# Kernel tuning notes

Hardware: AMD Instinct MI355X
Metric: run time of the kernel (lower is better)

Reference implementation:

```python
import jax, jax.numpy as jnp
import numpy as np

B, S, H = 2, 2048, 2048
N_HEADS = 16
HEAD_DIM = H // N_HEADS


def setup_inputs() -> dict:
    key = jax.random.key(0)
    k1, k2, k3 = jax.random.split(key, 3)
    # Xavier-uniform-ish init for weights, zeros for biases (matches _init_weights)
    lim_in = float(np.sqrt(6.0 / (H + 3 * H)))
    lim_out = float(np.sqrt(6.0 / (H + H)))
    return {
        "hidden_states": jax.random.normal(k1, (B, S, H), dtype=jnp.float32),
        "W_in": jax.random.uniform(k2, (3 * H, H), jnp.float32, -lim_in, lim_in),
        "b_in": jnp.zeros((3 * H,), jnp.float32),
        "W_out": jax.random.uniform(k3, (H, H), jnp.float32, -lim_out, lim_out),
        "b_out": jnp.zeros((H,), jnp.float32),
    }


def reference(hidden_states, W_in, b_in, W_out, b_out):
    b, s, h = hidden_states.shape
    qkv = hidden_states @ W_in.T + b_in  # [B,S,3H]
    q, k, v = jnp.split(qkv, 3, axis=-1)
    # [B,S,H] -> [B,N,S,D]
    def to_heads(x):
        return x.reshape(b, s, N_HEADS, HEAD_DIM).transpose(0, 2, 1, 3)
    q, k, v = to_heads(q), to_heads(k), to_heads(v)
    scale = HEAD_DIM ** -0.5
    scores = jnp.einsum("bnqd,bnkd->bnqk", q, k) * scale  # [B,N,S,S]
    causal = jnp.triu(jnp.ones((s, s), dtype=bool), k=1)
    scores = jnp.where(causal, -jnp.inf, scores)
    weights = jax.nn.softmax(scores, axis=-1)
    attn = jnp.einsum("bnqk,bnkd->bnqd", weights, v)  # [B,N,S,D]
    attn = attn.transpose(0, 2, 1, 3).reshape(b, s, h)
    return attn @ W_out.T + b_out
```

## Files before the change

kernel.cpp:

```cpp
#include <hip/hip_runtime.h>
#include <cstdint>

typedef __bf16 bf16x8 __attribute__((ext_vector_type(8)));
typedef __bf16 bf16x4 __attribute__((ext_vector_type(4)));
typedef float  f32x4  __attribute__((ext_vector_type(4)));

__device__ __forceinline__ void lds_load16(const void* g, void* l) {
  __builtin_amdgcn_global_load_lds(
      (const __attribute__((address_space(1))) unsigned int*)g,
      (__attribute__((address_space(3))) unsigned int*)l, 16, 0, 0);
}

__device__ __forceinline__ float grp16_max(float v) {
  v = fmaxf(v, __shfl_xor(v, 1));
  v = fmaxf(v, __shfl_xor(v, 2));
  v = fmaxf(v, __shfl_xor(v, 4));
  v = fmaxf(v, __shfl_xor(v, 8));
  return v;
}
__device__ __forceinline__ float grp16_sum(float v) {
  v += __shfl_xor(v, 1);
  v += __shfl_xor(v, 2);
  v += __shfl_xor(v, 4);
  v += __shfl_xor(v, 8);
  return v;
}

__global__ void f2bf_kernel(const float* __restrict__ in, __bf16* __restrict__ out, int n4) {
  int i = blockIdx.x * blockDim.x + threadIdx.x;
  if (i >= n4) return;
  const float4 v = reinterpret_cast<const float4*>(in)[i];
  bf16x4 o;
  o[0] = (__bf16)v.x; o[1] = (__bf16)v.y; o[2] = (__bf16)v.z; o[3] = (__bf16)v.w;
  reinterpret_cast<bf16x4*>(out)[i] = o;
}

template <int EPI>
__global__ __launch_bounds__(256)
void gemm_bt(const __bf16* __restrict__ A, const __bf16* __restrict__ Bm,
             int M, int N, int K, const float* __restrict__ bias,
             __bf16* __restrict__ qo, __bf16* __restrict__ ko, __bf16* __restrict__ vo,
             float* __restrict__ co)
{
  __shared__ __align__(16) __bf16 As[128 * 32];
  __shared__ __align__(16) __bf16 Bs[128 * 32];
  const int t = threadIdx.x;
  const int lane = t & 63, w = t >> 6;
  const int g = lane >> 4, r16 = lane & 15;
  const int tM = blockIdx.y * 128, tN = blockIdx.x * 128;
  const int wrow = (w >> 1) * 64, wcol = (w & 1) * 64;

  f32x4 acc[4][4] = {};
  const char* Ag = (const char*)A + (size_t)tM * K * 2;
  const char* Bg = (const char*)Bm + (size_t)tN * K * 2;
  const int ldb = K * 2;

  for (int k0 = 0; k0 < K; k0 += 32) {
    const char* Ak = Ag + (size_t)k0 * 2;
    const char* Bk = Bg + (size_t)k0 * 2;
#pragma unroll
    for (int it = 0; it < 2; it++) {
      int o = it * 4096 + t * 16;
      lds_load16(Ak + (size_t)(o >> 6) * ldb + (o & 63), (char*)As + o);
    }
#pragma unroll
    for (int it = 0; it < 2; it++) {
      int o = it * 4096 + t * 16;
      lds_load16(Bk + (size_t)(o >> 6) * ldb + (o & 63), (char*)Bs + o);
    }
    __syncthreads();
    bf16x8 af[4], bfr[4];
#pragma unroll
    for (int i = 0; i < 4; i++) af[i]  = *(const bf16x8*)&As[(wrow + i * 16 + r16) * 32 + g * 8];
#pragma unroll
    for (int i = 0; i < 4; i++) bfr[i] = *(const bf16x8*)&Bs[(wcol + i * 16 + r16) * 32 + g * 8];
#pragma unroll
    for (int i = 0; i < 4; i++)
#pragma unroll
      for (int j = 0; j < 4; j++)
        acc[i][j] = __builtin_amdgcn_mfma_f32_16x16x32_bf16(af[i], bfr[j], acc[i][j], 0, 0, 0);
    __syncthreads();
  }

  if (EPI == 0) {
#pragma unroll
    for (int j = 0; j < 4; j++) {
      int col = tN + wcol + j * 16 + r16;
      float bv = bias[col];
      int which = col >> 11;
      int f = col & 2047;
      int head = f >> 7, dd = f & 127;
      if (which == 2) {
#pragma unroll
        for (int i = 0; i < 4; i++) {
#pragma unroll
          for (int r = 0; r < 4; r++) {
            int m = tM + wrow + i * 16 + g * 4 + r;
            int bb = m >> 11, s = m & 2047;
            vo[((size_t)(bb * 16 + head) * 128 + dd) * 2048 + s] = (__bf16)(acc[i][j][r] + bv);
          }
        }
      } else {
        __bf16* dst = (which == 0) ? qo : ko;
        float sc = (which == 0) ? 0.12751757f : 1.0f;
#pragma unroll
        for (int i = 0; i < 4; i++) {
#pragma unroll
          for (int r = 0; r < 4; r++) {
            int m = tM + wrow + i * 16 + g * 4 + r;
            int bb = m >> 11, s = m & 2047;
            dst[((size_t)(bb * 16 + head) * 2048 + s) * 128 + dd] = (__bf16)((acc[i][j][r] + bv) * sc);
          }
        }
      }
    }
  } else {
#pragma unroll
    for (int j = 0; j < 4; j++) {
      int col = tN + wcol + j * 16 + r16;
      float bv = bias[col];
#pragma unroll
      for (int i = 0; i < 4; i++) {
#pragma unroll
        for (int r = 0; r < 4; r++) {
          int m = tM + wrow + i * 16 + g * 4 + r;
          co[(size_t)m * N + col] = acc[i][j][r] + bv;
        }
      }
    }
  }
}

__global__ __launch_bounds__(256)
void attn_kernel(const __bf16* __restrict__ Qb, const __bf16* __restrict__ Kb,
                 const __bf16* __restrict__ Vb, __bf16* __restrict__ Ob)
{
  const int pi = blockIdx.x;
  const int bh = blockIdx.y;
  const int b = bh >> 4, head = bh & 15;
  const int t = threadIdx.x, lane = t & 63, w = t >> 6;
  const int g = lane >> 4, r16 = lane & 15;

  __shared__ __align__(16) __bf16 Ks[2][64 * 128];
  __shared__ __align__(16) __bf16 Vs[2][128 * 64];
  __shared__ __align__(16) __bf16 Ps[4][16 * 72];

  const int qiS = pi, qiL = 31 - pi;
  const int q0S = qiS * 64, q0L = qiL * 64;

  const size_t hoff = (size_t)bh * 2048 * 128;
  const char* Kt0 = (const char*)(Kb + hoff);
  const char* Vt0 = (const char*)(Vb + hoff);

  bf16x8 qfL[4], qfS[4];
  {
    const __bf16* qp = Qb + hoff + (size_t)(q0L + w * 16 + r16) * 128 + g * 8;
#pragma unroll
    for (int ks = 0; ks < 4; ks++) qfL[ks] = *(const bf16x8*)(qp + ks * 32);
    const __bf16* qp2 = Qb + hoff + (size_t)(q0S + w * 16 + r16) * 128 + g * 8;
#pragma unroll
    for (int ks = 0; ks < 4; ks++) qfS[ks] = *(const bf16x8*)(qp2 + ks * 32);
  }

  f32x4 oL[8] = {}, oS[8] = {};
  float mL[4], lL[4], mS[4], lS[4];
#pragma unroll
  for (int r = 0; r < 4; r++) { mL[r] = -1e30f; lL[r] = 0.f; mS[r] = -1e30f; lS[r] = 0.f; }

#define STAGE(bb_, kt_) do {                                                   \
  const char* kg_ = Kt0 + (size_t)(kt_) * 16384;                               \
  const char* vg_ = Vt0 + (size_t)(kt_) * 128;                                 \
  _Pragma("unroll")                                                            \
  for (int it = 0; it < 4; it++) {                                             \
    int o = it * 4096 + t * 16;                                                \
    int swz = o ^ (((o >> 8) & 7) << 4);                                       \
    lds_load16(kg_ + swz, (char*)Ks[bb_] + o);                                 \
  }                                                                            \
  _Pragma("unroll")                                                            \
  for (int it = 0; it < 4; it++) {                                             \
    int o = it * 4096 + t * 16;                                                \
    int swz = o ^ (((o >> 7) & 7) << 4);                                       \
    lds_load16(vg_ + (size_t)(swz >> 7) * 4096 + (swz & 127), (char*)Vs[bb_] + o); \
  }                                                                            \
} while (0)

#define TILE_COMPUTE(qfX, oX, mX, lX, q0X, isDiag, bb_) do {                   \
  f32x4 sf[4];                                                                 \
  _Pragma("unroll")                                                            \
  for (int ni = 0; ni < 4; ni++) {                                             \
    f32x4 a = {};                                                              \
    _Pragma("unroll")                                                          \
    for (int ks = 0; ks < 4; ks++) {                                           \
      int row = ni * 16 + r16;                                                 \
      int off = (row * 256 + (ks * 32 + g * 8) * 2) ^ ((row & 7) << 4);        \
      bf16x8 kf = *(const bf16x8*)((const char*)Ks[bb_] + off);                \
      a = __builtin_amdgcn_mfma_f32_16x16x32_bf16(qfX[ks], kf, a, 0, 0, 0);    \
    }                                                                          \
    sf[ni] = a;                                                                \
  }                                                                            \
  if (isDiag) {                                                                \
    _Pragma("unroll")                                                          \
    for (int ni = 0; ni < 4; ni++) {                                           \
      int kg2 = kt * 64 + ni * 16 + r16;                                       \
      _Pragma("unroll")                                                        \
      for (int r = 0; r < 4; r++) {                                            \
        int qg = q0X + w * 16 + g * 4 + r;                                     \
        if (kg2 > qg) sf[ni][r] = -1e30f;                                      \
      }                                                                        \
    }                                                                          \
  }                                                                            \
  _Pragma("unroll")                                                            \
  for (int r = 0; r < 4; r++) {                                                \
    float mx = fmaxf(fmaxf(sf[0][r], sf[1][r]), fmaxf(sf[2][r], sf[3][r]));    \
    mx = grp16_max(mx);                                                        \
    float mn = fmaxf(mX[r], mx);                                               \
    float alpha = __builtin_amdgcn_exp2f(mX[r] - mn);                          \
    float ps = 0.f;                                                            \
    _Pragma("unroll")                                                          \
    for (int ni = 0; ni < 4; ni++) {                                           \
      float p = __builtin_amdgcn_exp2f(sf[ni][r] - mn);                        \
      sf[ni][r] = p; ps += p;                                                  \
    }                                                                          \
    ps = grp16_sum(ps);                                                        \
    lX[r] = lX[r] * alpha + ps;                                                \
    mX[r] = mn;                                                                \
    _Pragma("unroll")                                                          \
    for (int di = 0; di < 8; di++) oX[di][r] *= alpha;                         \
  }                                                                            \
  _Pragma("unroll")                                                            \
  for (int ni = 0; ni < 4; ni++)                                               \
    _Pragma("unroll")                                                          \
    for (int r = 0; r < 4; r++)                                                \
      Ps[w][(g * 4 + r) * 72 + ni * 16 + r16] = (__bf16)sf[ni][r];             \
  _Pragma("unroll")                                                            \
  for (int ks2 = 0; ks2 < 2; ks2++) {                                          \
    bf16x8 pa = *(const bf16x8*)&Ps[w][r16 * 72 + ks2 * 32 + g * 8];           \
    _Pragma("unroll")                                                          \
    for (int di = 0; di < 8; di++) {                                           \
      int d_ = di * 16 + r16;                                                  \
      int off = ((d_ << 7) + (ks2 * 32 + g * 8) * 2) ^ ((d_ & 7) << 4);        \
      bf16x8 vf = *(const bf16x8*)((const char*)Vs[bb_] + off);                \
      oX[di] = __builtin_amdgcn_mfma_f32_16x16x32_bf16(pa, vf, oX[di], 0, 0, 0); \
    }                                                                          \
  }                                                                            \
} while (0)

  STAGE(0, 0);
  __syncthreads();

  for (int kt = 0; kt <= qiL; ++kt) {
    const int bb = kt & 1;
    if (kt < qiL) STAGE(bb ^ 1, kt + 1);
    TILE_COMPUTE(qfL, oL, mL, lL, q0L, (kt == qiL), bb);
    if (kt <= qiS) TILE_COMPUTE(qfS, oS, mS, lS, q0S, (kt == qiS), bb);
    __syncthreads();
  }

#undef STAGE
#undef TILE_COMPUTE

#pragma unroll
  for (int r = 0; r < 4; r++) {
    float invL = 1.0f / lL[r];
    size_t rowL = ((size_t)b * 2048 + q0L + w * 16 + g * 4 + r) * 2048 + head * 128 + r16;
#pragma unroll
    for (int di = 0; di < 8; di++)
      Ob[rowL + di * 16] = (__bf16)(oL[di][r] * invL);
    float invS = 1.0f / lS[r];
    size_t rowS = ((size_t)b * 2048 + q0S + w * 16 + g * 4 + r) * 2048 + head * 128 + r16;
#pragma unroll
    for (int di = 0; di < 8; di++)
      Ob[rowS + di * 16] = (__bf16)(oS[di][r] * invS);
  }
}

extern "C" void kernel_launch(void* const* d_in, const int* in_sizes, int n_in,
                              void* d_out, int out_size, void* d_ws, size_t ws_size,
                              hipStream_t stream) {
  const float* X  = (const float*)d_in[0];
  const float* Wi = (const float*)d_in[1];
  const float* bi = (const float*)d_in[2];
  const float* Wo = (const float*)d_in[3];
  const float* bo = (const float*)d_in[4];
  float* out = (float*)d_out;

  char* p = (char*)d_ws;
  auto alloc = [&](size_t bytes) {
    char* r = p;
    p += (bytes + 255) & ~(size_t)255;
    return r;
  };
  __bf16* Xb  = (__bf16*)alloc((size_t)4096 * 2048 * 2);
  __bf16* Wib = (__bf16*)alloc((size_t)6144 * 2048 * 2);
  __bf16* Wob = (__bf16*)alloc((size_t)2048 * 2048 * 2);
  __bf16* Qb  = (__bf16*)alloc((size_t)32 * 2048 * 128 * 2);
  __bf16* Kb  = (__bf16*)alloc((size_t)32 * 2048 * 128 * 2);
  __bf16* Vb  = (__bf16*)alloc((size_t)32 * 2048 * 128 * 2);
  __bf16* Ab  = (__bf16*)alloc((size_t)4096 * 2048 * 2);

  {
    int n4 = 4096 * 2048 / 4;
    f2bf_kernel<<<(n4 + 255) / 256, 256, 0, stream>>>(X, Xb, n4);
  }
  {
    int n4 = 6144 * 2048 / 4;
    f2bf_kernel<<<(n4 + 255) / 256, 256, 0, stream>>>(Wi, Wib, n4);
  }
  {
    int n4 = 2048 * 2048 / 4;
    f2bf_kernel<<<(n4 + 255) / 256, 256, 0, stream>>>(Wo, Wob, n4);
  }

  gemm_bt<0><<<dim3(48, 32), 256, 0, stream>>>(Xb, Wib, 4096, 6144, 2048, bi,
                                               Qb, Kb, Vb, nullptr);
  attn_kernel<<<dim3(16, 32), 256, 0, stream>>>(Qb, Kb, Vb, Ab);
  gemm_bt<1><<<dim3(16, 32), 256, 0, stream>>>(Ab, Wob, 4096, 2048, 2048, bo,
                                               nullptr, nullptr, nullptr, out);
}
```

Baseline: 489.8 us.

## Add 256x256 ping-pong QKV GEMM, swizzle output GEMM LDS, raise MFMA priority

Replaces the QKV projection GEMM with a dedicated 256x256-tile kernel. It uses 512 threads, 128KB of double-buffered LDS, an XOR swizzle, split half-tile staging interleaved with MFMA phases and s_setprio, and a grouped block-index swizzle for L2 locality. The output GEMM gets an XOR swizzle on its LDS layout to reduce bank conflicts. The attention kernel raises wave priority around its MFMA sections. The aim is higher MFMA utilisation and less LDS and memory stall. The cost is more complex barrier and waitcnt logic and only one block per CU.

```diff
diff --git a/kernel.cpp b/kernel.cpp
--- a/kernel.cpp
+++ b/kernel.cpp
@@ -10,6 +10,8 @@
       (const __attribute__((address_space(1))) unsigned int*)g,
       (__attribute__((address_space(3))) unsigned int*)l, 16, 0, 0);
 }
+
+#define BAR() do { asm volatile("" ::: "memory"); __builtin_amdgcn_s_barrier(); asm volatile("" ::: "memory"); } while (0)
 
 __device__ __forceinline__ float grp16_max(float v) {
   v = fmaxf(v, __shfl_xor(v, 1));
@@ -35,12 +37,180 @@
   reinterpret_cast<bf16x4*>(out)[i] = o;
 }
 
-template <int EPI>
+__global__ __launch_bounds__(512, 1)
+void gemm256_qkv(const __bf16* __restrict__ A, const __bf16* __restrict__ Bm,
+                 const float* __restrict__ bias,
+                 __bf16* __restrict__ qo, __bf16* __restrict__ ko, __bf16* __restrict__ vo)
+{
+  constexpr int K = 2048, NT = K / 64;
+  __shared__ __align__(16) char lds8[131072];
+
+  const int t = threadIdx.x;
+  const int lane = t & 63, w = t >> 6;
+  const int g = lane >> 4, r16 = lane & 15;
+  const int wm = w >> 2, wn = w & 3;
+
+  const int bid = blockIdx.x;
+  const int swz = (bid & 7) * 48 + (bid >> 3);
+  const int tM = (swz & 15) * 256;
+  const int tN = (swz >> 4) * 256;
+
+  const char* Ag = (const char*)A + (size_t)tM * K * 2;
+  const char* Bg = (const char*)Bm + (size_t)tN * K * 2;
+  const int ld = K * 2;
+
+  auto STAGE_HALF = [&](int X, int h, int tb, int ktg) {
+#pragma unroll
+    for (int i = 0; i < 2; i++) {
+      int o = i * 8192 + t * 16;
+      int rl = o >> 7;
+      int inrow = (o & 127) ^ ((rl & 7) << 4);
+      const char* src = (X ? Bg : Ag) + (size_t)(h * 128 + rl) * ld + (size_t)ktg * 128 + inrow;
+      lds_load16(src, lds8 + tb * 65536 + X * 32768 + h * 16384 + o);
+    }
+  };
+
+  const int xorv = (r16 & 7) << 4;
+  const int aoff0 = (g * 16) ^ xorv;
+
+  f32x4 acc[8][4] = {};
+  bf16x8 af[8][2];
+  bf16x8 bfm[2][2];
+
+  STAGE_HALF(0, 0, 0, 0); STAGE_HALF(0, 1, 0, 0);
+  STAGE_HALF(1, 0, 0, 0); STAGE_HALF(1, 1, 0, 0);
+  STAGE_HALF(0, 0, 1, 1); STAGE_HALF(0, 1, 1, 1);
+  asm volatile("s_waitcnt vmcnt(4)" ::: "memory");
+  __builtin_amdgcn_s_barrier();
+
+  for (int kt = 0; kt < NT; ++kt) {
+    const int cb = kt & 1;
+    const char* aT = lds8 + cb * 65536;
+    const char* bT = aT + 32768;
+    const int arow = (wm * 128 + r16) * 128;
+    const int brow = (wn * 64 + r16) * 128;
+
+#pragma unroll
+    for (int mf = 0; mf < 4; mf++) {
+#pragma unroll
+      for (int ks = 0; ks < 2; ks++)
+        af[mf][ks] = *(const bf16x8*)(aT + arow + mf * 2048 + (aoff0 ^ (ks * 64)));
+    }
+#pragma unroll
+    for (int nf = 0; nf < 2; nf++) {
+#pragma unroll
+      for (int ks = 0; ks < 2; ks++)
+        bfm[nf][ks] = *(const bf16x8*)(bT + brow + nf * 2048 + (aoff0 ^ (ks * 64)));
+    }
+    if (kt + 1 < NT) STAGE_HALF(1, 0, cb ^ 1, kt + 1);
+    BAR();
+    __builtin_amdgcn_s_setprio(1);
+#pragma unroll
+    for (int mf = 0; mf < 4; mf++)
+#pragma unroll
+      for (int nf = 0; nf < 2; nf++)
+#pragma unroll
+        for (int ks = 0; ks < 2; ks++)
+          acc[mf][nf] = __builtin_amdgcn_mfma_f32_16x16x32_bf16(af[mf][ks], bfm[nf][ks], acc[mf][nf], 0, 0, 0);
+    __builtin_amdgcn_s_setprio(0);
+    BAR();
+
+#pragma unroll
+    for (int mf = 4; mf < 8; mf++) {
+#pragma unroll
+      for (int ks = 0; ks < 2; ks++)
+        af[mf][ks] = *(const bf16x8*)(aT + arow + mf * 2048 + (aoff0 ^ (ks * 64)));
+    }
+#pragma unroll
+    for (int nf = 0; nf < 2; nf++) {
+#pragma unroll
+      for (int ks = 0; ks < 2; ks++)
+        bfm[nf][ks] = *(const bf16x8*)(bT + brow + (nf + 2) * 2048 + (aoff0 ^ (ks * 64)));
+    }
+    if (kt + 1 < NT) STAGE_HALF(1, 1, cb ^ 1, kt + 1);
+    BAR();
+    __builtin_amdgcn_s_setprio(1);
+#pragma unroll
+    for (int mf = 4; mf < 8; mf++)
+#pragma unroll
+      for (int nf = 0; nf < 2; nf++)
+#pragma unroll
+        for (int ks = 0; ks < 2; ks++)
+          acc[mf][nf + 2] = __builtin_amdgcn_mfma_f32_16x16x32_bf16(af[mf][ks], bfm[nf][ks], acc[mf][nf + 2], 0, 0, 0);
+    __builtin_amdgcn_s_setprio(0);
+    BAR();
+
+    if (kt + 2 < NT) STAGE_HALF(0, 0, cb, kt + 2);
+    BAR();
+    __builtin_amdgcn_s_setprio(1);
+#pragma unroll
+    for (int mf = 0; mf < 4; mf++)
+#pragma unroll
+      for (int nf = 0; nf < 2; nf++)
+#pragma unroll
+        for (int ks = 0; ks < 2; ks++)
+          acc[mf][nf + 2] = __builtin_amdgcn_mfma_f32_16x16x32_bf16(af[mf][ks], bfm[nf][ks], acc[mf][nf + 2], 0, 0, 0);
+    __builtin_amdgcn_s_setprio(0);
+    BAR();
+
+#pragma unroll
+    for (int nf = 0; nf < 2; nf++) {
+#pragma unroll
+      for (int ks = 0; ks < 2; ks++)
+        bfm[nf][ks] = *(const bf16x8*)(bT + brow + nf * 2048 + (aoff0 ^ (ks * 64)));
+    }
+    if (kt + 2 < NT) STAGE_HALF(0, 1, cb, kt + 2);
+    BAR();
+    __builtin_amdgcn_s_setprio(1);
+#pragma unroll
+    for (int mf = 4; mf < 8; mf++)
+#pragma unroll
+      for (int nf = 0; nf < 2; nf++)
+#pragma unroll
+        for (int ks = 0; ks < 2; ks++)
+          acc[mf][nf] = __builtin_amdgcn_mfma_f32_16x16x32_bf16(af[mf][ks], bfm[nf][ks], acc[mf][nf], 0, 0, 0);
+    __builtin_amdgcn_s_setprio(0);
+    if (kt + 2 < NT) { asm volatile("s_waitcnt vmcnt(4)" ::: "memory"); }
+    else             { asm volatile("s_waitcnt vmcnt(0)" ::: "memory"); }
+    BAR();
+  }
+
+#pragma unroll
+  for (int nf = 0; nf < 4; nf++) {
+    int col = tN + wn * 64 + nf * 16 + r16;
+    float bv = bias[col];
+    int which = col >> 11;
+    int f = col & 2047;
+    int head = f >> 7, dd = f & 127;
+    if (which == 2) {
+#pragma unroll
+      for (int mf = 0; mf < 8; mf++) {
+#pragma unroll
+        for (int r = 0; r < 4; r++) {
+          int m = tM + wm * 128 + mf * 16 + g * 4 + r;
+          int bb2 = m >> 11, s = m & 2047;
+          vo[((size_t)(bb2 * 16 + head) * 128 + dd) * 2048 + s] = (__bf16)(acc[mf][nf][r] + bv);
+        }
+      }
+    } else {
+      __bf16* dst = (which == 0) ? qo : ko;
+      float sc = (which == 0) ? 0.12751757f : 1.0f;
+#pragma unroll
+      for (int mf = 0; mf < 8; mf++) {
+#pragma unroll
+        for (int r = 0; r < 4; r++) {
+          int m = tM + wm * 128 + mf * 16 + g * 4 + r;
+          int bb2 = m >> 11, s = m & 2047;
+          dst[((size_t)(bb2 * 16 + head) * 2048 + s) * 128 + dd] = (__bf16)((acc[mf][nf][r] + bv) * sc);
+        }
+      }
+    }
+  }
+}
+
 __global__ __launch_bounds__(256)
-void gemm_bt(const __bf16* __restrict__ A, const __bf16* __restrict__ Bm,
-             int M, int N, int K, const float* __restrict__ bias,
-             __bf16* __restrict__ qo, __bf16* __restrict__ ko, __bf16* __restrict__ vo,
-             float* __restrict__ co)
+void gemm_bt_f32(const __bf16* __restrict__ A, const __bf16* __restrict__ Bm,
+                 int M, int N, int K, const float* __restrict__ bias, float* __restrict__ co)
 {
   __shared__ __align__(16) __bf16 As[128 * 32];
   __shared__ __align__(16) __bf16 Bs[128 * 32];
@@ -54,6 +224,7 @@
   const char* Ag = (const char*)A + (size_t)tM * K * 2;
   const char* Bg = (const char*)Bm + (size_t)tN * K * 2;
   const int ldb = K * 2;
+  const int soff = ((r16 & 3) << 4);
 
   for (int k0 = 0; k0 < K; k0 += 32) {
     const char* Ak = Ag + (size_t)k0 * 2;
@@ -61,19 +232,25 @@
 #pragma unroll
     for (int it = 0; it < 2; it++) {
       int o = it * 4096 + t * 16;
-      lds_load16(Ak + (size_t)(o >> 6) * ldb + (o & 63), (char*)As + o);
+      int rl = o >> 6;
+      int inrow = (o & 63) ^ ((rl & 3) << 4);
+      lds_load16(Ak + (size_t)rl * ldb + inrow, (char*)As + o);
     }
 #pragma unroll
     for (int it = 0; it < 2; it++) {
       int o = it * 4096 + t * 16;
-      lds_load16(Bk + (size_t)(o >> 6) * ldb + (o & 63), (char*)Bs + o);
+      int rl = o >> 6;
+      int inrow = (o & 63) ^ ((rl & 3) << 4);
+      lds_load16(Bk + (size_t)rl * ldb + inrow, (char*)Bs + o);
     }
     __syncthreads();
     bf16x8 af[4], bfr[4];
 #pragma unroll
-    for (int i = 0; i < 4; i++) af[i]  = *(const bf16x8*)&As[(wrow + i * 16 + r16) * 32 + g * 8];
-#pragma unroll
-    for (int i = 0; i < 4; i++) bfr[i] = *(const bf16x8*)&Bs[(wcol + i * 16 + r16) * 32 + g * 8];
+    for (int i = 0; i < 4; i++)
+      af[i] = *(const bf16x8*)((const char*)As + (wrow + i * 16 + r16) * 64 + ((g * 16) ^ soff));
+#pragma unroll
+    for (int i = 0; i < 4; i++)
+      bfr[i] = *(const bf16x8*)((const char*)Bs + (wcol + i * 16 + r16) * 64 + ((g * 16) ^ soff));
 #pragma unroll
     for (int i = 0; i < 4; i++)
 #pragma unroll
@@ -82,50 +259,16 @@
     __syncthreads();
   }
 
-  if (EPI == 0) {
-#pragma unroll
-    for (int j = 0; j < 4; j++) {
-      int col = tN + wcol + j * 16 + r16;
-      float bv = bias[col];
-      int which = col >> 11;
-      int f = col & 2047;
-      int head = f >> 7, dd = f & 127;
-      if (which == 2) {
-#pragma unroll
-        for (int i = 0; i < 4; i++) {
-#pragma unroll
-          for (int r = 0; r < 4; r++) {
-            int m = tM + wrow + i * 16 + g * 4 + r;
-            int bb = m >> 11, s = m & 2047;
-            vo[((size_t)(bb * 16 + head) * 128 + dd) * 2048 + s] = (__bf16)(acc[i][j][r] + bv);
-          }
-        }
-      } else {
-        __bf16* dst = (which == 0) ? qo : ko;
-        float sc = (which == 0) ? 0.12751757f : 1.0f;
-#pragma unroll
-        for (int i = 0; i < 4; i++) {
-#pragma unroll
-          for (int r = 0; r < 4; r++) {
-            int m = tM + wrow + i * 16 + g * 4 + r;
-            int bb = m >> 11, s = m & 2047;
-            dst[((size_t)(bb * 16 + head) * 2048 + s) * 128 + dd] = (__bf16)((acc[i][j][r] + bv) * sc);
-          }
-        }
-      }
-    }
-  } else {
-#pragma unroll
-    for (int j = 0; j < 4; j++) {
-      int col = tN + wcol + j * 16 + r16;
-      float bv = bias[col];
-#pragma unroll
-      for (int i = 0; i < 4; i++) {
-#pragma unroll
-        for (int r = 0; r < 4; r++) {
-          int m = tM + wrow + i * 16 + g * 4 + r;
-          co[(size_t)m * N + col] = acc[i][j][r] + bv;
-        }
+#pragma unroll
+  for (int j = 0; j < 4; j++) {
+    int col = tN + wcol + j * 16 + r16;
+    float bv = bias[col];
+#pragma unroll
+    for (int i = 0; i < 4; i++) {
+#pragma unroll
+      for (int r = 0; r < 4; r++) {
+        int m = tM + wrow + i * 16 + g * 4 + r;
+        co[(size_t)m * N + col] = acc[i][j][r] + bv;
       }
     }
   }
@@ -186,6 +329,7 @@
 
 #define TILE_COMPUTE(qfX, oX, mX, lX, q0X, isDiag, bb_) do {                   \
   f32x4 sf[4];                                                                 \
+  __builtin_amdgcn_s_setprio(1);                                               \
   _Pragma("unroll")                                                            \
   for (int ni = 0; ni < 4; ni++) {                                             \
     f32x4 a = {};                                                              \
@@ -198,6 +342,7 @@
     }                                                                          \
     sf[ni] = a;                                                                \
   }                                                                            \
+  __builtin_amdgcn_s_setprio(0);                                               \
   if (isDiag) {                                                                \
     _Pragma("unroll")                                                          \
     for (int ni = 0; ni < 4; ni++) {                                           \
@@ -232,6 +377,7 @@
     _Pragma("unroll")                                                          \
     for (int r = 0; r < 4; r++)                                                \
       Ps[w][(g * 4 + r) * 72 + ni * 16 + r16] = (__bf16)sf[ni][r];             \
+  __builtin_amdgcn_s_setprio(1);                                               \
   _Pragma("unroll")                                                            \
   for (int ks2 = 0; ks2 < 2; ks2++) {                                          \
     bf16x8 pa = *(const bf16x8*)&Ps[w][r16 * 72 + ks2 * 32 + g * 8];           \
@@ -243,6 +389,7 @@
       oX[di] = __builtin_amdgcn_mfma_f32_16x16x32_bf16(pa, vf, oX[di], 0, 0, 0); \
     }                                                                          \
   }                                                                            \
+  __builtin_amdgcn_s_setprio(0);                                               \
 } while (0)
 
   STAGE(0, 0);
@@ -311,9 +458,7 @@
     f2bf_kernel<<<(n4 + 255) / 256, 256, 0, stream>>>(Wo, Wob, n4);
   }
 
-  gemm_bt<0><<<dim3(48, 32), 256, 0, stream>>>(Xb, Wib, 4096, 6144, 2048, bi,
-                                               Qb, Kb, Vb, nullptr);
+  gemm256_qkv<<<dim3(384), 512, 0, stream>>>(Xb, Wib, bi, Qb, Kb, Vb);
   attn_kernel<<<dim3(16, 32), 256, 0, stream>>>(Qb, Kb, Vb, Ab);
-  gemm_bt<1><<<dim3(16, 32), 256, 0, stream>>>(Ab, Wob, 4096, 2048, 2048, bo,
-                                               nullptr, nullptr, nullptr, out);
-}
+  gemm_bt_f32<<<dim3(16, 32), 256, 0, stream>>>(Ab, Wob, 4096, 2048, 2048, bo, out);
+}
```

Result: faster. 471.6 us (-3.7%).
